# Optimization experiments

Measured on AMD Instinct MI355X. Metric: run time of the kernel, lower is better.

The kernel has to match this reference:

```python
import jax, jax.numpy as jnp
from jax import lax
import numpy as np

B, HI, WI = 8, 56, 56
HO, WO = HI // 2, WI // 2
DIN, DOUT = 96, 192
N_IN, N_OUT = HI * WI, HO * WO
HD = 32
NH = DOUT // HD
H2, W2, N2 = HO, WO, HO * WO
NA_W = 7
NUM_ITERS, DEPTH = 3, 2


def _build_group_tables():
    # M_loc: 0 inside 3x3 output window around each input token, -1e4 elsewhere
    # qidx: which of the 9 relative offsets maps (input i -> output j); -1 outside window
    mask = np.full((N_IN, N_OUT), -1e4, np.float32)
    idx = np.full((N_IN, N_OUT), -1, np.int64)
    rr, cc = np.meshgrid(np.arange(HI), np.arange(WI), indexing='ij')
    rr, cc = rr.ravel(), cc.ravel()
    r0, c0 = rr // 2, cc // 2
    ii = np.arange(N_IN)
    offs = [(dr, dc) for dr in (-1, 0, 1) for dc in (-1, 0, 1)]
    for kk, (dr, dc) in enumerate(offs):
        oi = np.clip(r0 + dr, 0, HO - 1) * WO + np.clip(c0 + dc, 0, WO - 1)
        mask[ii, oi] = 0.0
        idx[ii, oi] = kk
    # torch rpb[-1] == rpb[8]; emulate negative indexing with %9
    return jnp.asarray(mask), jnp.asarray(idx % 9)

M_LOC, QIDX = _build_group_tables()


def _rope_tables(n, d):
    inv = 1.0 / (10000.0 ** (np.arange(0, d, 2, dtype=np.float32) / d))
    ang = np.outer(np.arange(n, dtype=np.float32), inv)
    return jnp.asarray(np.cos(ang), jnp.float32), jnp.asarray(np.sin(ang), jnp.float32)

ROPE_COS, ROPE_SIN = _rope_tables(N2, HD)


def _na_idx(n, w):
    # NATTEN-style shifted windows: center clamped so the window stays in-bounds
    half = w // 2
    c = np.clip(np.arange(n), half, n - 1 - half)
    return jnp.asarray(c[:, None] + np.arange(-half, half + 1)[None, :])

NB_R = _na_idx(H2, NA_W)
NB_C = _na_idx(W2, NA_W)


def _ln(x, g, b):
    m = x.mean(-1, keepdims=True)
    v = ((x - m) ** 2).mean(-1, keepdims=True)
    return (x - m) / jnp.sqrt(v + 1e-5) * g + b


def _rope(t):  # t: [B, N, heads, head_dim]
    b, n, h, d = t.shape
    tr = t.reshape(b, n, h, d // 2, 2)
    x0, x1 = tr[..., 0], tr[..., 1]
    c = ROPE_COS[None, :, None, :]
    s = ROPE_SIN[None, :, None, :]
    return jnp.stack([x0 * c - x1 * s, x1 * c + x0 * s], -1).reshape(b, n, h, d)


def _forward(x, seed_conv_w, q_proj_w, k_proj_w, v_proj_w, g_ln_in_g, g_ln_in_b, g_ln_out_g, g_ln_out_b, g_ln_attn_g, g_ln_attn_b, g_ln_mlp_g, g_ln_mlp_b, g_mlp_w1, g_mlp_b1, g_mlp_w2, g_mlp_b2, tau, rpb, blk_ln1_g, blk_ln1_b, blk_ln2_g, blk_ln2_b, blk_qkv_w, blk_proj_w, blk_proj_b, blk_mlp_w1, blk_mlp_b1, blk_mlp_w2, blk_mlp_b2):
    b = x.shape[0]
    # ---- SparseGroupingLayer (local/sparse path), eval mode ----
    xc = x.transpose(0, 2, 1).reshape(b, DIN, HI, WI)
    seed = lax.conv_general_dilated(xc, seed_conv_w, (2, 2), ((1, 1), (1, 1)), dimension_numbers=('NCHW', 'OIHW', 'NCHW'))
    x_out = _ln(seed.reshape(b, DOUT, N_OUT).transpose(0, 2, 1), g_ln_out_g, g_ln_out_b)
    xn = _ln(x, g_ln_in_g, g_ln_in_b)
    k = xn @ k_proj_w.T
    v = xn @ v_proj_w.T
    bias = rpb[QIDX] + M_LOC  # [N_in, N_out]
    scale = jnp.exp(tau[0])
    for _ in range(NUM_ITERS):
        q = _ln(x_out, g_ln_out_g, g_ln_out_b) @ q_proj_w.T  # [B, N_out, dim_in]
        logits = jnp.einsum('bnd,bmd->bnm', k, q) * scale + bias[None]
        a_ups = jax.nn.softmax(logits, -1)
        a_down = a_ups / (a_ups.sum(1, keepdims=True) + 1e-8)
        upd = jnp.einsum('bnm,bnd->bmd', a_down, v)
        x_out = x_out + _ln(upd, g_ln_attn_g, g_ln_attn_b)
        h = jax.nn.gelu(x_out @ g_mlp_w1.T + g_mlp_b1, approximate=False) @ g_mlp_w2.T + g_mlp_b2
        x_out = x_out + _ln(h, g_ln_mlp_g, g_ln_mlp_b)
    # ---- SeNaTraBlocks: neighborhood attention (window=7) + RoPE, eval mode ----
    rows = NB_R[:, None, :, None]
    cols = NB_C[None, :, None, :]
    for i in range(DEPTH):
        xb = _ln(x_out, blk_ln1_g[i], blk_ln1_b[i])
        qkv = (xb @ blk_qkv_w[i].T).reshape(b, N2, 3, NH, HD)
        q = _rope(qkv[:, :, 0]).transpose(0, 2, 1, 3).reshape(b, NH, H2, W2, HD)
        kk = _rope(qkv[:, :, 1]).transpose(0, 2, 1, 3).reshape(b, NH, H2, W2, HD)
        vv = qkv[:, :, 2].transpose(0, 2, 1, 3).reshape(b, NH, H2, W2, HD)
        kn = kk[:, :, rows, cols].reshape(b, NH, H2, W2, NA_W * NA_W, HD)
        vn = vv[:, :, rows, cols].reshape(b, NH, H2, W2, NA_W * NA_W, HD)
        att = jnp.einsum('bhijd,bhijkd->bhijk', q, kn) * (HD ** -0.5)
        att = jax.nn.softmax(att, -1)
        o = jnp.einsum('bhijk,bhijkd->bhijd', att, vn)
        o = o.reshape(b, NH, N2, HD).transpose(0, 2, 1, 3).reshape(b, N2, DOUT)
        x_out = x_out + (o @ blk_proj_w[i].T + blk_proj_b[i])
        xb = _ln(x_out, blk_ln2_g[i], blk_ln2_b[i])
        h = jax.nn.gelu(xb @ blk_mlp_w1[i].T + blk_mlp_b1[i], approximate=False) @ blk_mlp_w2[i].T + blk_mlp_b2[i]
        x_out = x_out + h
    return x_out


def setup_inputs() -> dict:
    key = jax.random.key(0)
    ks = jax.random.split(key, 12)
    hid_g, hid_b = 2 * DOUT, 3 * DOUT
    def rn(k, shape, s=0.02):
        return jax.random.normal(k, shape, jnp.float32) * s
    return {
        'x': jax.random.normal(ks[0], (B, N_IN, DIN), jnp.float32),
        'seed_conv_w': rn(ks[1], (DOUT, DIN, 3, 3), 0.05),
        'q_proj_w': rn(ks[2], (DIN, DOUT)),
        'k_proj_w': rn(ks[3], (DIN, DIN)),
        'v_proj_w': rn(ks[4], (DOUT, DIN)),
        'g_ln_in_g': jnp.ones((DIN,), jnp.float32), 'g_ln_in_b': jnp.zeros((DIN,), jnp.float32),
        'g_ln_out_g': jnp.ones((DOUT,), jnp.float32), 'g_ln_out_b': jnp.zeros((DOUT,), jnp.float32),
        'g_ln_attn_g': jnp.ones((DOUT,), jnp.float32), 'g_ln_attn_b': jnp.zeros((DOUT,), jnp.float32),
        'g_ln_mlp_g': jnp.ones((DOUT,), jnp.float32), 'g_ln_mlp_b': jnp.zeros((DOUT,), jnp.float32),
        'g_mlp_w1': rn(ks[5], (hid_g, DOUT)), 'g_mlp_b1': jnp.zeros((hid_g,), jnp.float32),
        'g_mlp_w2': rn(ks[6], (DOUT, hid_g)), 'g_mlp_b2': jnp.zeros((DOUT,), jnp.float32),
        'tau': jnp.array([float(np.log(DIN ** -0.5))], jnp.float32),
        'rpb': rn(ks[7], (9,)),
        'blk_ln1_g': jnp.ones((DEPTH, DOUT), jnp.float32), 'blk_ln1_b': jnp.zeros((DEPTH, DOUT), jnp.float32),
        'blk_ln2_g': jnp.ones((DEPTH, DOUT), jnp.float32), 'blk_ln2_b': jnp.zeros((DEPTH, DOUT), jnp.float32),
        'blk_qkv_w': rn(ks[8], (DEPTH, 3 * DOUT, DOUT)),
        'blk_proj_w': rn(ks[9], (DEPTH, DOUT, DOUT)), 'blk_proj_b': jnp.zeros((DEPTH, DOUT), jnp.float32),
        'blk_mlp_w1': rn(ks[10], (DEPTH, hid_b, DOUT)), 'blk_mlp_b1': jnp.zeros((DEPTH, hid_b), jnp.float32),
        'blk_mlp_w2': rn(ks[11], (DEPTH, DOUT, hid_b)), 'blk_mlp_b2': jnp.zeros((DEPTH, DOUT), jnp.float32),
    }


def reference(x, seed_conv_w, q_proj_w, k_proj_w, v_proj_w, g_ln_in_g, g_ln_in_b, g_ln_out_g, g_ln_out_b, g_ln_attn_g, g_ln_attn_b, g_ln_mlp_g, g_ln_mlp_b, g_mlp_w1, g_mlp_b1, g_mlp_w2, g_mlp_b2, tau, rpb, blk_ln1_g, blk_ln1_b, blk_ln2_g, blk_ln2_b, blk_qkv_w, blk_proj_w, blk_proj_b, blk_mlp_w1, blk_mlp_b1, blk_mlp_w2, blk_mlp_b2):
    return _forward(x, seed_conv_w, q_proj_w, k_proj_w, v_proj_w, g_ln_in_g, g_ln_in_b, g_ln_out_g, g_ln_out_b, g_ln_attn_g, g_ln_attn_b, g_ln_mlp_g, g_ln_mlp_b, g_mlp_w1, g_mlp_b1, g_mlp_w2, g_mlp_b2, tau, rpb, blk_ln1_g, blk_ln1_b, blk_ln2_g, blk_ln2_b, blk_qkv_w, blk_proj_w, blk_proj_b, blk_mlp_w1, blk_mlp_b1, blk_mlp_w2, blk_mlp_b2)
```

## Files before the change

kernel.cpp:

```cpp
#include <hip/hip_runtime.h>
#include <hip/hip_bf16.h>

#define DEV __device__ __forceinline__

typedef __attribute__((ext_vector_type(8))) short short8;
typedef __attribute__((ext_vector_type(4))) float f32x4;

DEV unsigned short f2b(float f) {
  union { float f; unsigned u; } v; v.f = f;
  unsigned r = v.u + 0x7FFFu + ((v.u >> 16) & 1u);
  return (unsigned short)(r >> 16);
}
DEV float b2f16(unsigned short b) {
  union { unsigned u; float f; } v; v.u = ((unsigned)b) << 16;
  return v.f;
}
DEV void tsplit(float v, short& h, short& l) {
  union { float f; unsigned u; } c; c.f = v;
  unsigned short hu = (unsigned short)(c.u >> 16);
  union { unsigned u; float f; } hb; hb.u = (unsigned)hu << 16;
  union { float f; unsigned u; } c2; c2.f = v - hb.f;
  h = (short)hu; l = (short)(c2.u >> 16);
}

__global__ void k_castw(const float* __restrict__ s0, const float* __restrict__ s1,
    const float* __restrict__ s2, const float* __restrict__ s3,
    const float* __restrict__ s4, const float* __restrict__ s5,
    const float* __restrict__ s6, const float* __restrict__ s7,
    const float* __restrict__ s8, const float* __restrict__ s9,
    short* __restrict__ dh, short* __restrict__ dl) {
  int idx = blockIdx.x * 256 + threadIdx.x;
  if (idx >= 1096704) return;
  float v;
  if (idx < 165888) {
    int co = idx / 864, rem = idx % 864;
    int k9 = rem / 96, ci = rem % 96;
    v = s0[co * 864 + ci * 9 + k9];
  } else {
    const float* src; int base;
    if      (idx < 175104) { src = s1; base = 165888; }
    else if (idx < 193536) { src = s2; base = 175104; }
    else if (idx < 211968) { src = s3; base = 193536; }
    else if (idx < 285696) { src = s4; base = 211968; }
    else if (idx < 359424) { src = s5; base = 285696; }
    else if (idx < 580608) { src = s6; base = 359424; }
    else if (idx < 654336) { src = s7; base = 580608; }
    else if (idx < 875520) { src = s8; base = 654336; }
    else                   { src = s9; base = 875520; }
    v = src[idx - base];
  }
  unsigned short h = f2b(v);
  dh[idx] = (short)h;
  dl[idx] = (short)f2b(v - b2f16(h));
}

__global__ void k_rope(float* ct, float* st) {
  int idx = blockIdx.x * 256 + threadIdx.x;
  if (idx >= 784 * 16) return;
  int n = idx >> 4, j = idx & 15;
  float inv = powf(10000.f, -(float)(2 * j) / 32.f);
  float ang = (float)n * inv;
  ct[idx] = cosf(ang);
  st[idx] = sinf(ang);
}

template<int D>
__global__ __launch_bounds__(256) void k_lnstat(const float* __restrict__ in,
    float2* __restrict__ stats, int M) {
  int tok = blockIdx.x * 4 + (threadIdx.x >> 6);
  int l = threadIdx.x & 63;
  if (tok >= M) return;
  const float* row = in + (size_t)tok * D;
  constexpr int E = (D + 63) / 64;
  float s = 0.f, s2 = 0.f;
#pragma unroll
  for (int e = 0; e < E; ++e) {
    int i = e * 64 + l;
    float x = (i < D) ? row[i] : 0.f;
    s += x; s2 += x * x;
  }
  for (int off = 32; off; off >>= 1) { s += __shfl_xor(s, off); s2 += __shfl_xor(s2, off); }
  float mean = s / D, var = s2 / D - mean * mean;
  if (l == 0) stats[tok] = make_float2(mean, rsqrtf(var + 1e-5f));
}

template<int ADD>
__global__ __launch_bounds__(256) void k_ln_epi(const float* __restrict__ raw,
    const float* __restrict__ g, const float* __restrict__ b,
    float* __restrict__ out, float2* __restrict__ stats, int M) {
  int tok = blockIdx.x * 4 + (threadIdx.x >> 6);
  int l = threadIdx.x & 63;
  if (tok >= M) return;
  const float* row = raw + (size_t)tok * 192;
  float v[3];
  float s = 0.f, s2 = 0.f;
#pragma unroll
  for (int e = 0; e < 3; ++e) {
    float x = row[e * 64 + l];
    v[e] = x; s += x; s2 += x * x;
  }
  for (int off = 32; off; off >>= 1) { s += __shfl_xor(s, off); s2 += __shfl_xor(s2, off); }
  float mean = s / 192.f, var = s2 / 192.f - mean * mean;
  float rstd = rsqrtf(var + 1e-5f);
  float* orow = out + (size_t)tok * 192;
  float t = 0.f, t2 = 0.f;
#pragma unroll
  for (int e = 0; e < 3; ++e) {
    int i = e * 64 + l;
    float r = (v[e] - mean) * rstd * g[i] + b[i];
    float nv = ADD ? (orow[i] + r) : r;
    orow[i] = nv;
    t += nv; t2 += nv * nv;
  }
  for (int off = 32; off; off >>= 1) { t += __shfl_xor(t, off); t2 += __shfl_xor(t2, off); }
  float m2 = t / 192.f, v2 = t2 / 192.f - m2 * m2;
  if (l == 0) stats[tok] = make_float2(m2, rsqrtf(v2 + 1e-5f));
}

template<int EPI, int CONV, int LNS>
__global__ __launch_bounds__(128) void k_mgemm(
    const float* __restrict__ A, const short* __restrict__ WH,
    const short* __restrict__ WL, const float* __restrict__ bias,
    float* __restrict__ C, int M, int N, int K,
    const float2* __restrict__ lnstats, const float* __restrict__ lng,
    const float* __restrict__ lnb,
    const float* __restrict__ ct, const float* __restrict__ st,
    float* __restrict__ o1, float* __restrict__ o2, float* __restrict__ o3) {
  __shared__ short AsH[32][40], AsL[32][40];
  __shared__ short BsH[64][40], BsL[64][40];
  int t = threadIdx.x;
  int m0 = blockIdx.x * 32, n0 = blockIdx.y * 64;
  int sr = t >> 2, sq = (t & 3) * 8;
  int sr2 = t >> 1, sq2 = (t & 1) * 16;
  int lane = t & 63, w = t >> 6;
  int fr = lane & 15, fq = lane >> 4;
  float2 lst = make_float2(0.f, 1.f);
  if (LNS) lst = lnstats[m0 + sr];
  f32x4 acc[2][2];
#pragma unroll
  for (int i = 0; i < 2; ++i)
#pragma unroll
    for (int j = 0; j < 2; ++j) acc[i][j] = (f32x4){0.f, 0.f, 0.f, 0.f};

  for (int kt = 0; kt < K; kt += 32) {
    short8 vh, vl;
    if (CONV) {
      int m = m0 + sr;
      int b = m / 784, rm = m % 784, ho = rm / 28, wo = rm % 28;
      int k = kt + sq;
      int k9 = k / 96, ci0 = k % 96;
      int hi = 2 * ho - 1 + k9 / 3, wi = 2 * wo - 1 + k9 % 3;
      if (hi >= 0 && hi < 56 && wi >= 0 && wi < 56) {
        const float* src = &A[((size_t)b * 3136 + hi * 56 + wi) * 96 + ci0];
        float4 a0 = *(const float4*)src;
        float4 a1 = *(const float4*)(src + 4);
        float av[8] = {a0.x, a0.y, a0.z, a0.w, a1.x, a1.y, a1.z, a1.w};
#pragma unroll
        for (int j = 0; j < 8; ++j) { short h, l2; tsplit(av[j], h, l2); vh[j] = h; vl[j] = l2; }
      } else {
#pragma unroll
        for (int j = 0; j < 8; ++j) { vh[j] = 0; vl[j] = 0; }
      }
    } else {
      const float4 a0 = *(const float4*)&A[(size_t)(m0 + sr) * K + kt + sq];
      const float4 a1 = *(const float4*)&A[(size_t)(m0 + sr) * K + kt + sq + 4];
      float av[8] = {a0.x, a0.y, a0.z, a0.w, a1.x, a1.y, a1.z, a1.w};
#pragma unroll
      for (int j = 0; j < 8; ++j) {
        if (LNS) av[j] = (av[j] - lst.x) * lst.y * lng[kt + sq + j] + lnb[kt + sq + j];
        short h, l2; tsplit(av[j], h, l2); vh[j] = h; vl[j] = l2;
      }
    }
    *(short8*)&AsH[sr][sq] = vh;
    *(short8*)&AsL[sr][sq] = vl;
    {
      int n = n0 + sr2;
      if (n < N) {
        *(short8*)&BsH[sr2][sq2]     = *(const short8*)&WH[(size_t)n * K + kt + sq2];
        *(short8*)&BsH[sr2][sq2 + 8] = *(const short8*)&WH[(size_t)n * K + kt + sq2 + 8];
        *(short8*)&BsL[sr2][sq2]     = *(const short8*)&WL[(size_t)n * K + kt + sq2];
        *(short8*)&BsL[sr2][sq2 + 8] = *(const short8*)&WL[(size_t)n * K + kt + sq2 + 8];
      } else {
        short8 z = {0, 0, 0, 0, 0, 0, 0, 0};
        *(short8*)&BsH[sr2][sq2] = z; *(short8*)&BsH[sr2][sq2 + 8] = z;
        *(short8*)&BsL[sr2][sq2] = z; *(short8*)&BsL[sr2][sq2 + 8] = z;
      }
    }
    __syncthreads();
    short8 ah[2], al[2], bh[2], bl[2];
#pragma unroll
    for (int s = 0; s < 2; ++s) {
      ah[s] = *(const short8*)&AsH[s * 16 + fr][fq * 8];
      al[s] = *(const short8*)&AsL[s * 16 + fr][fq * 8];
      bh[s] = *(const short8*)&BsH[w * 32 + s * 16 + fr][fq * 8];
      bl[s] = *(const short8*)&BsL[w * 32 + s * 16 + fr][fq * 8];
    }
#pragma unroll
    for (int i = 0; i < 2; ++i)
#pragma unroll
      for (int j = 0; j < 2; ++j) {
        acc[i][j] = __builtin_amdgcn_mfma_f32_16x16x32_bf16(ah[i], bh[j], acc[i][j], 0, 0, 0);
        acc[i][j] = __builtin_amdgcn_mfma_f32_16x16x32_bf16(ah[i], bl[j], acc[i][j], 0, 0, 0);
        acc[i][j] = __builtin_amdgcn_mfma_f32_16x16x32_bf16(al[i], bh[j], acc[i][j], 0, 0, 0);
      }
    __syncthreads();
  }
#pragma unroll
  for (int i = 0; i < 2; ++i) {
#pragma unroll
    for (int j = 0; j < 2; ++j) {
      int n = n0 + w * 32 + j * 16 + fr;
#pragma unroll
      for (int r = 0; r < 4; ++r) {
        int m = m0 + i * 16 + fq * 4 + r;
        float v = acc[i][j][r];
        float pa = 0.f;
        if (EPI == 3) pa = __shfl_xor(v, 1);
        if (n >= N) continue;
        if (bias) v += bias[n];
        if (EPI == 1) v = 0.5f * v * (1.f + erff(v * 0.70710678118654752f));
        if (EPI == 3) {
          int sec = n / 192, d = n % 192, h = d / 32, dh = d % 32;
          int b = m / 784, mm = m % 784;
          float val;
          if (sec < 2) {
            int jj = dh >> 1;
            float cc = ct[mm * 16 + jj], ss = st[mm * 16 + jj];
            val = (dh & 1) ? (v * cc + pa * ss) : (v * cc - pa * ss);
          } else val = v;
          float* dst = (sec == 0) ? o1 : ((sec == 1) ? o2 : o3);
          dst[(((size_t)b * 6 + h) * 784 + mm) * 32 + dh] = val;
        } else if (EPI == 5) {
          if (n < 96) o1[(size_t)m * 96 + n] = v;
          else        o2[(size_t)m * 192 + (n - 96)] = v;
        } else if (EPI == 2) {
          C[(size_t)m * N + n] += v;
        } else {
          C[(size_t)m * N + n] = v;
        }
      }
    }
  }
}

__global__ __launch_bounds__(256) void k_pass1(const float* __restrict__ kk,
    const float* __restrict__ q, const float* __restrict__ rpb,
    const float* __restrict__ tau, float* __restrict__ M, float* __restrict__ Z) {
  int tok = blockIdx.x * 4 + (threadIdx.x >> 6);
  int l = threadIdx.x & 63;
  int b = tok / 3136, n = tok % 3136;
  int r = n / 56, c = n % 56, r0 = r >> 1, c0 = c >> 1;
  int oi[9]; bool keep[9];
#pragma unroll
  for (int kki = 0; kki < 9; ++kki) {
    int dr = kki / 3 - 1, dc = kki % 3 - 1;
    int rr = min(max(r0 + dr, 0), 27), cc = min(max(c0 + dc, 0), 27);
    oi[kki] = rr * 28 + cc;
  }
#pragma unroll
  for (int kki = 0; kki < 9; ++kki) {
    bool kp = true;
#pragma unroll
    for (int k2 = kki + 1; k2 < 9; ++k2) if (oi[k2] == oi[kki]) kp = false;
    keep[kki] = kp;
  }
  float scale = expf(tau[0]);
  const float* kr = kk + (size_t)tok * 96;
  float k0 = kr[l];
  float k1 = (l < 32) ? kr[64 + l] : 0.f;
  float lg[9];
  float mx = -1e30f;
#pragma unroll
  for (int kki = 0; kki < 9; ++kki) {
    if (keep[kki]) {
      const float* qr = q + ((size_t)b * 784 + oi[kki]) * 96;
      float part = k0 * qr[l];
      if (l < 32) part += k1 * qr[64 + l];
      for (int off = 32; off; off >>= 1) part += __shfl_xor(part, off);
      lg[kki] = part * scale + rpb[kki];
      mx = fmaxf(mx, lg[kki]);
    } else lg[kki] = -1e30f;
  }
  float z = 0.f;
#pragma unroll
  for (int kki = 0; kki < 9; ++kki) if (keep[kki]) z += expf(lg[kki] - mx);
  if (l == 0) { M[tok] = mx; Z[tok] = z; }
}

__global__ __launch_bounds__(192) void k_pass2(const float* __restrict__ kk,
    const float* __restrict__ q, const float* __restrict__ vv,
    const float* __restrict__ M, const float* __restrict__ Z,
    const float* __restrict__ rpb, const float* __restrict__ tau,
    const float* __restrict__ g, const float* __restrict__ bb, float* __restrict__ xout) {
  int bid = blockIdx.x;
  int blk = (bid & 7) * 784 + (bid >> 3);
  int b = blk / 784, m = blk % 784;
  int r2 = m / 28, c2 = m % 28;
  int r0lo = (r2 == 0) ? 0 : r2 - 1, r0hi = (r2 == 27) ? 27 : r2 + 1;
  int c0lo = (c2 == 0) ? 0 : c2 - 1, c0hi = (c2 == 27) ? 27 : c2 + 1;
  int nrow = 2 * (r0hi - r0lo + 1), ncol = 2 * (c0hi - c0lo + 1);
  int cnt = nrow * ncol;
  __shared__ float qm[96], p[36];
  __shared__ int nlist[36];
  __shared__ float2 red[192];
  int t = threadIdx.x;
  if (t < 96) qm[t] = q[(size_t)blk * 96 + t];
  __syncthreads();
  if (t < cnt) {
    int rr = 2 * r0lo + t / ncol, cc = 2 * c0lo + t % ncol;
    int n = rr * 56 + cc, rr0 = rr >> 1, cc0 = cc >> 1;
    int kkf = 0;
#pragma unroll
    for (int kki = 0; kki < 9; ++kki) {
      int dr = kki / 3 - 1, dc = kki % 3 - 1;
      int ra = min(max(rr0 + dr, 0), 27), ca = min(max(cc0 + dc, 0), 27);
      if (ra == r2 && ca == c2) kkf = kki;
    }
    const float* krow = kk + ((size_t)b * 3136 + n) * 96;
    float d = 0.f;
    for (int i = 0; i < 96; ++i) d += krow[i] * qm[i];
    float scale = expf(tau[0]);
    float lg = d * scale + rpb[kkf];
    size_t idn = (size_t)b * 3136 + n;
    p[t] = expf(lg - M[idn]) / Z[idn];
    nlist[t] = n;
  }
  __syncthreads();
  float denom = 0.f;
  for (int jn = 0; jn < cnt; ++jn) denom += p[jn];
  float acc = 0.f;
  for (int jn = 0; jn < cnt; ++jn)
    acc += p[jn] * vv[((size_t)b * 3136 + nlist[jn]) * 192 + t];
  float upd = acc / (denom + 1e-8f);
  red[t] = make_float2(upd, upd * upd);
  __syncthreads();
  for (int s = 128; s > 0; s >>= 1) {
    if (t < s && t + s < 192) { red[t].x += red[t + s].x; red[t].y += red[t + s].y; }
    __syncthreads();
  }
  float mean = red[0].x / 192.f, var = red[0].y / 192.f - mean * mean;
  float rstd = rsqrtf(var + 1e-5f);
  xout[(size_t)blk * 192 + t] += (upd - mean) * rstd * g[t] + bb[t];
}

__global__ __launch_bounds__(256) void k_attn(const float* __restrict__ q3,
    const float* __restrict__ k3, const float* __restrict__ v3, float* __restrict__ ob) {
  int bid = blockIdx.x;
  int swz = (bid & 7) * 1176 + (bid >> 3);
  int unit = swz * 4 + (threadIdx.x >> 6);
  int l = threadIdx.x & 63;
  int b = unit / (6 * 784), rem = unit % (6 * 784), h = rem / 784, m = rem % 784;
  int i = m / 28, j = m % 28;
  int ib = min(max(i, 3), 24) - 3, jb = min(max(j, 3), 24) - 3;
  size_t base = (size_t)(b * 6 + h) * 784 * 32;
  const float4* q4 = (const float4*)(q3 + base + (size_t)m * 32);
  float4 qv[8];
#pragma unroll
  for (int e = 0; e < 8; ++e) qv[e] = q4[e];
  float logit = -1e30f;
  if (l < 49) {
    int nk = (ib + l / 7) * 28 + (jb + l % 7);
    const float4* k4 = (const float4*)(k3 + base + (size_t)nk * 32);
    float a = 0.f;
#pragma unroll
    for (int e = 0; e < 8; ++e) {
      float4 kv = k4[e];
      a += qv[e].x * kv.x + qv[e].y * kv.y + qv[e].z * kv.z + qv[e].w * kv.w;
    }
    logit = a * 0.17677669529663687f;
  }
  float mx = logit;
  for (int off = 32; off; off >>= 1) mx = fmaxf(mx, __shfl_xor(mx, off));
  float p = (l < 49) ? expf(logit - mx) : 0.f;
  int half = l >> 5, d = l & 31;
  const float* vb = v3 + base + d;
  int rowbase = ib * 28 + jb;
  float accA = 0.f, accB = 0.f, psum = 0.f;
  int pbits = __float_as_int(p);
#pragma unroll
  for (int kk2 = 0; kk2 < 25; ++kk2) {
    const int k0c = kk2;
    const int k1c = (kk2 + 25 <= 48) ? kk2 + 25 : 48;
    float pk0 = __int_as_float(__builtin_amdgcn_readlane(pbits, k0c));
    float pk1 = (kk2 < 24) ? __int_as_float(__builtin_amdgcn_readlane(pbits, k1c)) : 0.f;
    const int c0 = (k0c / 7) * 28 + (k0c % 7);
    const int c1 = (k1c / 7) * 28 + (k1c % 7);
    float pk = half ? pk1 : pk0;
    int nk = rowbase + (half ? c1 : c0);
    psum += pk;
    float term = pk * vb[(size_t)nk * 32];
    if (kk2 & 1) accB += term; else accA += term;
  }
  float acc = accA + accB;
  acc += __shfl_xor(acc, 32);
  psum += __shfl_xor(psum, 32);
  if (l < 32)
    ob[(((size_t)b * 784 + m) * 6 + h) * 32 + l] = acc / psum;
}

extern "C" void kernel_launch(void* const* d_in, const int* in_sizes, int n_in,
                              void* d_out, int out_size, void* d_ws, size_t ws_size,
                              hipStream_t stream) {
  (void)in_sizes; (void)n_in; (void)out_size; (void)ws_size;
  const float* x        = (const float*)d_in[0];
  const float* convw    = (const float*)d_in[1];
  const float* qw       = (const float*)d_in[2];
  const float* kw       = (const float*)d_in[3];
  const float* vw       = (const float*)d_in[4];
  const float* ln_in_g  = (const float*)d_in[5];
  const float* ln_in_b  = (const float*)d_in[6];
  const float* ln_out_g = (const float*)d_in[7];
  const float* ln_out_b = (const float*)d_in[8];
  const float* ln_at_g  = (const float*)d_in[9];
  const float* ln_at_b  = (const float*)d_in[10];
  const float* ln_ml_g  = (const float*)d_in[11];
  const float* ln_ml_b  = (const float*)d_in[12];
  const float* gw1      = (const float*)d_in[13];
  const float* gb1      = (const float*)d_in[14];
  const float* gw2      = (const float*)d_in[15];
  const float* gb2      = (const float*)d_in[16];
  const float* tau      = (const float*)d_in[17];
  const float* rpb      = (const float*)d_in[18];
  const float* bln1g    = (const float*)d_in[19];
  const float* bln1b    = (const float*)d_in[20];
  const float* bln2g    = (const float*)d_in[21];
  const float* bln2b    = (const float*)d_in[22];
  const float* bqkvw    = (const float*)d_in[23];
  const float* bprojw   = (const float*)d_in[24];
  const float* bprojb   = (const float*)d_in[25];
  const float* bmw1     = (const float*)d_in[26];
  const float* bmb1     = (const float*)d_in[27];
  const float* bmw2     = (const float*)d_in[28];
  const float* bmb2     = (const float*)d_in[29];

  float* XOUT = (float*)d_out;

  float* W = (float*)d_ws;
  size_t off = 0;
  float* Kb    = W + off; off += (size_t)25088 * 96;
  float* Vb    = W + off; off += (size_t)25088 * 192;
  float* Qb    = W + off; off += (size_t)6272 * 96;
  float* Mb    = W + off; off += (size_t)25088;
  float* Zb    = W + off; off += (size_t)25088;
  float* H1    = W + off; off += (size_t)6272 * 576;
  float* T2    = W + off; off += (size_t)6272 * 192;
  float* CT    = W + off; off += (size_t)784 * 16;
  float* ST    = W + off; off += (size_t)784 * 16;
  float2* S96  = (float2*)(W + off); off += (size_t)25088 * 2;
  float2* S192 = (float2*)(W + off); off += (size_t)6272 * 2;
  short* WBH   = (short*)(W + off); off += (size_t)548352 + 16;
  short* WBL   = (short*)(W + off); off += (size_t)548352 + 16;
  const size_t O_c = 0, O_k = 165888, O_v = 175104, O_q = 193536,
               O_g1 = 211968, O_g2 = 285696, O_qkv = 359424, O_p = 580608,
               O_m1 = 654336, O_m2 = 875520;
  (void)O_v;
  float* CRAW = T2;
  float* Q3 = Kb;
  float* K3 = Kb + (size_t)1204224;
  float* V3 = Vb;
  float* OB = Vb + (size_t)1204224;

  k_castw<<<4284, 256, 0, stream>>>(convw, kw, vw, qw, gw1, gw2, bqkvw, bprojw,
                                    bmw1, bmw2, WBH, WBL);
  k_rope<<<49, 256, 0, stream>>>(CT, ST);

  k_mgemm<0, 1, 0><<<dim3(196, 3), 128, 0, stream>>>(x, WBH + O_c, WBL + O_c, nullptr,
      CRAW, 6272, 192, 864, nullptr, nullptr, nullptr,
      nullptr, nullptr, nullptr, nullptr, nullptr);
  k_ln_epi<0><<<1568, 256, 0, stream>>>(CRAW, ln_out_g, ln_out_b, XOUT, S192, 6272);

  k_lnstat<96><<<6272, 256, 0, stream>>>(x, S96, 25088);
  k_mgemm<5, 0, 1><<<dim3(784, 5), 128, 0, stream>>>(x, WBH + O_k, WBL + O_k, nullptr,
      nullptr, 25088, 288, 96, S96, ln_in_g, ln_in_b,
      nullptr, nullptr, Kb, Vb, nullptr);

  for (int it = 0; it < 3; ++it) {
    k_mgemm<0, 0, 1><<<dim3(196, 2), 128, 0, stream>>>(XOUT, WBH + O_q, WBL + O_q, nullptr,
        Qb, 6272, 96, 192, S192, ln_out_g, ln_out_b,
        nullptr, nullptr, nullptr, nullptr, nullptr);
    k_pass1<<<6272, 256, 0, stream>>>(Kb, Qb, rpb, tau, Mb, Zb);
    k_pass2<<<6272, 192, 0, stream>>>(Kb, Qb, Vb, Mb, Zb, rpb, tau, ln_at_g, ln_at_b, XOUT);
    k_mgemm<1, 0, 0><<<dim3(196, 6), 128, 0, stream>>>(XOUT, WBH + O_g1, WBL + O_g1, gb1,
        H1, 6272, 384, 192, nullptr, nullptr, nullptr,
        nullptr, nullptr, nullptr, nullptr, nullptr);
    k_mgemm<0, 0, 0><<<dim3(196, 3), 128, 0, stream>>>(H1, WBH + O_g2, WBL + O_g2, gb2,
        T2, 6272, 192, 384, nullptr, nullptr, nullptr,
        nullptr, nullptr, nullptr, nullptr, nullptr);
    k_ln_epi<1><<<1568, 256, 0, stream>>>(T2, ln_ml_g, ln_ml_b, XOUT, S192, 6272);
  }

  for (int i = 0; i < 2; ++i) {
    if (i == 1) k_lnstat<192><<<1568, 256, 0, stream>>>(XOUT, S192, 6272);
    k_mgemm<3, 0, 1><<<dim3(196, 9), 128, 0, stream>>>(XOUT, WBH + O_qkv + (size_t)i * 110592,
        WBL + O_qkv + (size_t)i * 110592, nullptr,
        nullptr, 6272, 576, 192, S192, bln1g + (size_t)i * 192, bln1b + (size_t)i * 192,
        CT, ST, Q3, K3, V3);
    k_attn<<<9408, 256, 0, stream>>>(Q3, K3, V3, OB);
    k_mgemm<2, 0, 0><<<dim3(196, 3), 128, 0, stream>>>(OB, WBH + O_p + (size_t)i * 36864,
        WBL + O_p + (size_t)i * 36864, bprojb + (size_t)i * 192,
        XOUT, 6272, 192, 192, nullptr, nullptr, nullptr,
        nullptr, nullptr, nullptr, nullptr, nullptr);
    k_lnstat<192><<<1568, 256, 0, stream>>>(XOUT, S192, 6272);
    k_mgemm<1, 0, 1><<<dim3(196, 9), 128, 0, stream>>>(XOUT, WBH + O_m1 + (size_t)i * 110592,
        WBL + O_m1 + (size_t)i * 110592, bmb1 + (size_t)i * 576,
        H1, 6272, 576, 192, S192, bln2g + (size_t)i * 192, bln2b + (size_t)i * 192,
        nullptr, nullptr, nullptr, nullptr, nullptr);
    k_mgemm<2, 0, 0><<<dim3(196, 3), 128, 0, stream>>>(H1, WBH + O_m2 + (size_t)i * 110592,
        WBL + O_m2 + (size_t)i * 110592, bmb2 + (size_t)i * 192,
        XOUT, 6272, 192, 576, nullptr, nullptr, nullptr,
        nullptr, nullptr, nullptr, nullptr, nullptr);
  }
}
```

Before: 619.9 us.

## Precompute bf16 hi/lo split activations in producer epilogues instead of GEMM prologues

```diff
diff --git a/kernel.cpp b/kernel.cpp
--- a/kernel.cpp
+++ b/kernel.cpp
@@ -65,29 +65,42 @@
 }
 
 template<int D>
-__global__ __launch_bounds__(256) void k_lnstat(const float* __restrict__ in,
-    float2* __restrict__ stats, int M) {
+__global__ __launch_bounds__(256) void k_lnsplit(const float* __restrict__ in,
+    const float* __restrict__ g, const float* __restrict__ b,
+    short* __restrict__ xh, short* __restrict__ xl, int M) {
   int tok = blockIdx.x * 4 + (threadIdx.x >> 6);
   int l = threadIdx.x & 63;
   if (tok >= M) return;
   const float* row = in + (size_t)tok * D;
   constexpr int E = (D + 63) / 64;
+  float v[E];
   float s = 0.f, s2 = 0.f;
 #pragma unroll
   for (int e = 0; e < E; ++e) {
     int i = e * 64 + l;
     float x = (i < D) ? row[i] : 0.f;
-    s += x; s2 += x * x;
+    v[e] = x; s += x; s2 += x * x;
   }
   for (int off = 32; off; off >>= 1) { s += __shfl_xor(s, off); s2 += __shfl_xor(s2, off); }
   float mean = s / D, var = s2 / D - mean * mean;
-  if (l == 0) stats[tok] = make_float2(mean, rsqrtf(var + 1e-5f));
+  float rstd = rsqrtf(var + 1e-5f);
+#pragma unroll
+  for (int e = 0; e < E; ++e) {
+    int i = e * 64 + l;
+    if (i < D) {
+      float r = (v[e] - mean) * rstd * g[i] + b[i];
+      short h2, l2; tsplit(r, h2, l2);
+      xh[(size_t)tok * D + i] = h2;
+      xl[(size_t)tok * D + i] = l2;
+    }
+  }
 }
 
 template<int ADD>
 __global__ __launch_bounds__(256) void k_ln_epi(const float* __restrict__ raw,
     const float* __restrict__ g, const float* __restrict__ b,
-    float* __restrict__ out, float2* __restrict__ stats, int M) {
+    const float* __restrict__ eg, const float* __restrict__ eb,
+    float* __restrict__ out, short* __restrict__ xh, short* __restrict__ xl, int M) {
   int tok = blockIdx.x * 4 + (threadIdx.x >> 6);
   int l = threadIdx.x & 63;
   if (tok >= M) return;
@@ -103,29 +116,39 @@
   float mean = s / 192.f, var = s2 / 192.f - mean * mean;
   float rstd = rsqrtf(var + 1e-5f);
   float* orow = out + (size_t)tok * 192;
+  float nv[3];
   float t = 0.f, t2 = 0.f;
 #pragma unroll
   for (int e = 0; e < 3; ++e) {
     int i = e * 64 + l;
     float r = (v[e] - mean) * rstd * g[i] + b[i];
-    float nv = ADD ? (orow[i] + r) : r;
-    orow[i] = nv;
-    t += nv; t2 += nv * nv;
+    float x = ADD ? (orow[i] + r) : r;
+    orow[i] = x;
+    nv[e] = x;
+    t += x; t2 += x * x;
   }
   for (int off = 32; off; off >>= 1) { t += __shfl_xor(t, off); t2 += __shfl_xor(t2, off); }
   float m2 = t / 192.f, v2 = t2 / 192.f - m2 * m2;
-  if (l == 0) stats[tok] = make_float2(m2, rsqrtf(v2 + 1e-5f));
-}
-
-template<int EPI, int CONV, int LNS>
+  float rstd2 = rsqrtf(v2 + 1e-5f);
+#pragma unroll
+  for (int e = 0; e < 3; ++e) {
+    int i = e * 64 + l;
+    float r = (nv[e] - m2) * rstd2 * eg[i] + eb[i];
+    short h2, l2; tsplit(r, h2, l2);
+    xh[(size_t)tok * 192 + i] = h2;
+    xl[(size_t)tok * 192 + i] = l2;
+  }
+}
+
+template<int EPI, int SRC>
 __global__ __launch_bounds__(128) void k_mgemm(
-    const float* __restrict__ A, const short* __restrict__ WH,
+    const float* __restrict__ Aconv, const short* __restrict__ AH,
+    const short* __restrict__ AL, const short* __restrict__ WH,
     const short* __restrict__ WL, const float* __restrict__ bias,
     float* __restrict__ C, int M, int N, int K,
-    const float2* __restrict__ lnstats, const float* __restrict__ lng,
-    const float* __restrict__ lnb,
     const float* __restrict__ ct, const float* __restrict__ st,
-    float* __restrict__ o1, float* __restrict__ o2, float* __restrict__ o3) {
+    float* __restrict__ o1, float* __restrict__ o2, float* __restrict__ o3,
+    short* __restrict__ oh, short* __restrict__ ol) {
   __shared__ short AsH[32][40], AsL[32][40];
   __shared__ short BsH[64][40], BsL[64][40];
   int t = threadIdx.x;
@@ -134,8 +157,6 @@
   int sr2 = t >> 1, sq2 = (t & 1) * 16;
   int lane = t & 63, w = t >> 6;
   int fr = lane & 15, fq = lane >> 4;
-  float2 lst = make_float2(0.f, 1.f);
-  if (LNS) lst = lnstats[m0 + sr];
   f32x4 acc[2][2];
 #pragma unroll
   for (int i = 0; i < 2; ++i)
@@ -143,15 +164,18 @@
     for (int j = 0; j < 2; ++j) acc[i][j] = (f32x4){0.f, 0.f, 0.f, 0.f};
 
   for (int kt = 0; kt < K; kt += 32) {
-    short8 vh, vl;
-    if (CONV) {
+    if (SRC == 1) {
+      *(short8*)&AsH[sr][sq] = *(const short8*)&AH[(size_t)(m0 + sr) * K + kt + sq];
+      *(short8*)&AsL[sr][sq] = *(const short8*)&AL[(size_t)(m0 + sr) * K + kt + sq];
+    } else {
+      short8 vh, vl;
       int m = m0 + sr;
       int b = m / 784, rm = m % 784, ho = rm / 28, wo = rm % 28;
       int k = kt + sq;
       int k9 = k / 96, ci0 = k % 96;
       int hi = 2 * ho - 1 + k9 / 3, wi = 2 * wo - 1 + k9 % 3;
       if (hi >= 0 && hi < 56 && wi >= 0 && wi < 56) {
-        const float* src = &A[((size_t)b * 3136 + hi * 56 + wi) * 96 + ci0];
+        const float* src = &Aconv[((size_t)b * 3136 + hi * 56 + wi) * 96 + ci0];
         float4 a0 = *(const float4*)src;
         float4 a1 = *(const float4*)(src + 4);
         float av[8] = {a0.x, a0.y, a0.z, a0.w, a1.x, a1.y, a1.z, a1.w};
@@ -161,18 +185,9 @@
 #pragma unroll
         for (int j = 0; j < 8; ++j) { vh[j] = 0; vl[j] = 0; }
       }
-    } else {
-      const float4 a0 = *(const float4*)&A[(size_t)(m0 + sr) * K + kt + sq];
-      const float4 a1 = *(const float4*)&A[(size_t)(m0 + sr) * K + kt + sq + 4];
-      float av[8] = {a0.x, a0.y, a0.z, a0.w, a1.x, a1.y, a1.z, a1.w};
-#pragma unroll
-      for (int j = 0; j < 8; ++j) {
-        if (LNS) av[j] = (av[j] - lst.x) * lst.y * lng[kt + sq + j] + lnb[kt + sq + j];
-        short h, l2; tsplit(av[j], h, l2); vh[j] = h; vl[j] = l2;
-      }
-    }
-    *(short8*)&AsH[sr][sq] = vh;
-    *(short8*)&AsL[sr][sq] = vl;
+      *(short8*)&AsH[sr][sq] = vh;
+      *(short8*)&AsL[sr][sq] = vl;
+    }
     {
       int n = n0 + sr2;
       if (n < N) {
@@ -218,8 +233,12 @@
         if (EPI == 3) pa = __shfl_xor(v, 1);
         if (n >= N) continue;
         if (bias) v += bias[n];
-        if (EPI == 1) v = 0.5f * v * (1.f + erff(v * 0.70710678118654752f));
-        if (EPI == 3) {
+        if (EPI == 1) {
+          v = 0.5f * v * (1.f + erff(v * 0.70710678118654752f));
+          short h2, l2; tsplit(v, h2, l2);
+          oh[(size_t)m * N + n] = h2;
+          ol[(size_t)m * N + n] = l2;
+        } else if (EPI == 3) {
           int sec = n / 192, d = n % 192, h = d / 32, dh = d % 32;
           int b = m / 784, mm = m % 784;
           float val;
@@ -291,7 +310,8 @@
     const float* __restrict__ q, const float* __restrict__ vv,
     const float* __restrict__ M, const float* __restrict__ Z,
     const float* __restrict__ rpb, const float* __restrict__ tau,
-    const float* __restrict__ g, const float* __restrict__ bb, float* __restrict__ xout) {
+    const float* __restrict__ g, const float* __restrict__ bb,
+    float* __restrict__ xout, short* __restrict__ xh, short* __restrict__ xl) {
   int bid = blockIdx.x;
   int blk = (bid & 7) * 784 + (bid >> 3);
   int b = blk / 784, m = blk % 784;
@@ -340,11 +360,16 @@
   }
   float mean = red[0].x / 192.f, var = red[0].y / 192.f - mean * mean;
   float rstd = rsqrtf(var + 1e-5f);
-  xout[(size_t)blk * 192 + t] += (upd - mean) * rstd * g[t] + bb[t];
+  float nv = xout[(size_t)blk * 192 + t] + (upd - mean) * rstd * g[t] + bb[t];
+  xout[(size_t)blk * 192 + t] = nv;
+  short h2, l2; tsplit(nv, h2, l2);
+  xh[(size_t)blk * 192 + t] = h2;
+  xl[(size_t)blk * 192 + t] = l2;
 }
 
 __global__ __launch_bounds__(256) void k_attn(const float* __restrict__ q3,
-    const float* __restrict__ k3, const float* __restrict__ v3, float* __restrict__ ob) {
+    const float* __restrict__ k3, const float* __restrict__ v3,
+    short* __restrict__ obh, short* __restrict__ obl) {
   int bid = blockIdx.x;
   int swz = (bid & 7) * 1176 + (bid >> 3);
   int unit = swz * 4 + (threadIdx.x >> 6);
@@ -394,8 +419,13 @@
   float acc = accA + accB;
   acc += __shfl_xor(acc, 32);
   psum += __shfl_xor(psum, 32);
-  if (l < 32)
-    ob[(((size_t)b * 784 + m) * 6 + h) * 32 + l] = acc / psum;
+  if (l < 32) {
+    float o = acc / psum;
+    short h2, l2; tsplit(o, h2, l2);
+    size_t idx = (((size_t)b * 784 + m) * 6 + h) * 32 + l;
+    obh[idx] = h2;
+    obl[idx] = l2;
+  }
 }
 
 extern "C" void kernel_launch(void* const* d_in, const int* in_sizes, int n_in,
@@ -442,72 +472,82 @@
   float* Qb    = W + off; off += (size_t)6272 * 96;
   float* Mb    = W + off; off += (size_t)25088;
   float* Zb    = W + off; off += (size_t)25088;
-  float* H1    = W + off; off += (size_t)6272 * 576;
   float* T2    = W + off; off += (size_t)6272 * 192;
   float* CT    = W + off; off += (size_t)784 * 16;
   float* ST    = W + off; off += (size_t)784 * 16;
-  float2* S96  = (float2*)(W + off); off += (size_t)25088 * 2;
-  float2* S192 = (float2*)(W + off); off += (size_t)6272 * 2;
+  short* XH96  = (short*)(W + off); off += (size_t)25088 * 96 / 2;
+  short* XL96  = (short*)(W + off); off += (size_t)25088 * 96 / 2;
+  short* XH    = (short*)(W + off); off += (size_t)6272 * 192 / 2;
+  short* XL    = (short*)(W + off); off += (size_t)6272 * 192 / 2;
+  short* H1H   = (short*)(W + off); off += (size_t)6272 * 576 / 2;
+  short* H1L   = (short*)(W + off); off += (size_t)6272 * 576 / 2;
+  short* OBH   = (short*)(W + off); off += (size_t)6272 * 192 / 2;
+  short* OBL   = (short*)(W + off); off += (size_t)6272 * 192 / 2;
   short* WBH   = (short*)(W + off); off += (size_t)548352 + 16;
   short* WBL   = (short*)(W + off); off += (size_t)548352 + 16;
-  const size_t O_c = 0, O_k = 165888, O_v = 175104, O_q = 193536,
+  const size_t O_c = 0, O_k = 165888, O_q = 193536,
                O_g1 = 211968, O_g2 = 285696, O_qkv = 359424, O_p = 580608,
                O_m1 = 654336, O_m2 = 875520;
-  (void)O_v;
   float* CRAW = T2;
   float* Q3 = Kb;
   float* K3 = Kb + (size_t)1204224;
   float* V3 = Vb;
-  float* OB = Vb + (size_t)1204224;
 
   k_castw<<<4284, 256, 0, stream>>>(convw, kw, vw, qw, gw1, gw2, bqkvw, bprojw,
                                     bmw1, bmw2, WBH, WBL);
   k_rope<<<49, 256, 0, stream>>>(CT, ST);
 
-  k_mgemm<0, 1, 0><<<dim3(196, 3), 128, 0, stream>>>(x, WBH + O_c, WBL + O_c, nullptr,
-      CRAW, 6272, 192, 864, nullptr, nullptr, nullptr,
-      nullptr, nullptr, nullptr, nullptr, nullptr);
-  k_ln_epi<0><<<1568, 256, 0, stream>>>(CRAW, ln_out_g, ln_out_b, XOUT, S192, 6272);
-
-  k_lnstat<96><<<6272, 256, 0, stream>>>(x, S96, 25088);
-  k_mgemm<5, 0, 1><<<dim3(784, 5), 128, 0, stream>>>(x, WBH + O_k, WBL + O_k, nullptr,
-      nullptr, 25088, 288, 96, S96, ln_in_g, ln_in_b,
-      nullptr, nullptr, Kb, Vb, nullptr);
+  k_mgemm<0, 0><<<dim3(196, 3), 128, 0, stream>>>(x, nullptr, nullptr,
+      WBH + O_c, WBL + O_c, nullptr, CRAW, 6272, 192, 864,
+      nullptr, nullptr, nullptr, nullptr, nullptr, nullptr, nullptr);
+  k_ln_epi<0><<<1568, 256, 0, stream>>>(CRAW, ln_out_g, ln_out_b, ln_out_g, ln_out_b,
+                                        XOUT, XH, XL, 6272);
+
+  k_lnsplit<96><<<6272, 256, 0, stream>>>(x, ln_in_g, ln_in_b, XH96, XL96, 25088);
+  k_mgemm<5, 1><<<dim3(784, 5), 128, 0, stream>>>(nullptr, XH96, XL96,
+      WBH + O_k, WBL + O_k, nullptr, nullptr, 25088, 288, 96,
+      nullptr, nullptr, Kb, Vb, nullptr, nullptr, nullptr);
 
   for (int it = 0; it < 3; ++it) {
-    k_mgemm<0, 0, 1><<<dim3(196, 2), 128, 0, stream>>>(XOUT, WBH + O_q, WBL + O_q, nullptr,
-        Qb, 6272, 96, 192, S192, ln_out_g, ln_out_b,
-        nullptr, nullptr, nullptr, nullptr, nullptr);
+    k_mgemm<0, 1><<<dim3(196, 2), 128, 0, stream>>>(nullptr, XH, XL,
+        WBH + O_q, WBL + O_q, nullptr, Qb, 6272, 96, 192,
+        nullptr, nullptr, nullptr, nullptr, nullptr, nullptr, nullptr);
     k_pass1<<<6272, 256, 0, stream>>>(Kb, Qb, rpb, tau, Mb, Zb);
-    k_pass2<<<6272, 192, 0, stream>>>(Kb, Qb, Vb, Mb, Zb, rpb, tau, ln_at_g, ln_at_b, XOUT);
-    k_mgemm<1, 0, 0><<<dim3(196, 6), 128, 0, stream>>>(XOUT, WBH + O_g1, WBL + O_g1, gb1,
-        H1, 6272, 384, 192, nullptr, nullptr, nullptr,
-        nullptr, nullptr, nullptr, nullptr, nullptr);
-    k_mgemm<0, 0, 0><<<dim3(196, 3), 128, 0, stream>>>(H1, WBH + O_g2, WBL + O_g2, gb2,
-        T2, 6272, 192, 384, nullptr, nullptr, nullptr,
-        nullptr, nullptr, nullptr, nullptr, nullptr);
-    k_ln_epi<1><<<1568, 256, 0, stream>>>(T2, ln_ml_g, ln_ml_b, XOUT, S192, 6272);
+    k_pass2<<<6272, 192, 0, stream>>>(Kb, Qb, Vb, Mb, Zb, rpb, tau, ln_at_g, ln_at_b,
+                                      XOUT, XH, XL);
+    k_mgemm<1, 1><<<dim3(196, 6), 128, 0, stream>>>(nullptr, XH, XL,
+        WBH + O_g1, WBL + O_g1, gb1, nullptr, 6272, 384, 192,
+        nullptr, nullptr, nullptr, nullptr, nullptr, H1H, H1L);
+    k_mgemm<0, 1><<<dim3(196, 3), 128, 0, stream>>>(nullptr, H1H, H1L,
+        WBH + O_g2, WBL + O_g2, gb2, T2, 6272, 192, 384,
+        nullptr, nullptr, nullptr, nullptr, nullptr, nullptr, nullptr);
+    const float* eg = (it < 2) ? ln_out_g : bln1g;
+    const float* eb = (it < 2) ? ln_out_b : bln1b;
+    k_ln_epi<1><<<1568, 256, 0, stream>>>(T2, ln_ml_g, ln_ml_b, eg, eb,
+                                          XOUT, XH, XL, 6272);
   }
 
   for (int i = 0; i < 2; ++i) {
-    if (i == 1) k_lnstat<192><<<1568, 256, 0, stream>>>(XOUT, S192, 6272);
-    k_mgemm<3, 0, 1><<<dim3(196, 9), 128, 0, stream>>>(XOUT, WBH + O_qkv + (size_t)i * 110592,
-        WBL + O_qkv + (size_t)i * 110592, nullptr,
-        nullptr, 6272, 576, 192, S192, bln1g + (size_t)i * 192, bln1b + (size_t)i * 192,
-        CT, ST, Q3, K3, V3);
-    k_attn<<<9408, 256, 0, stream>>>(Q3, K3, V3, OB);
-    k_mgemm<2, 0, 0><<<dim3(196, 3), 128, 0, stream>>>(OB, WBH + O_p + (size_t)i * 36864,
-        WBL + O_p + (size_t)i * 36864, bprojb + (size_t)i * 192,
-        XOUT, 6272, 192, 192, nullptr, nullptr, nullptr,
-        nullptr, nullptr, nullptr, nullptr, nullptr);
-    k_lnstat<192><<<1568, 256, 0, stream>>>(XOUT, S192, 6272);
-    k_mgemm<1, 0, 1><<<dim3(196, 9), 128, 0, stream>>>(XOUT, WBH + O_m1 + (size_t)i * 110592,
-        WBL + O_m1 + (size_t)i * 110592, bmb1 + (size_t)i * 576,
-        H1, 6272, 576, 192, S192, bln2g + (size_t)i * 192, bln2b + (size_t)i * 192,
-        nullptr, nullptr, nullptr, nullptr, nullptr);
-    k_mgemm<2, 0, 0><<<dim3(196, 3), 128, 0, stream>>>(H1, WBH + O_m2 + (size_t)i * 110592,
-        WBL + O_m2 + (size_t)i * 110592, bmb2 + (size_t)i * 192,
-        XOUT, 6272, 192, 576, nullptr, nullptr, nullptr,
-        nullptr, nullptr, nullptr, nullptr, nullptr);
-  }
-}
+    k_mgemm<3, 1><<<dim3(196, 9), 128, 0, stream>>>(nullptr, XH, XL,
+        WBH + O_qkv + (size_t)i * 110592, WBL + O_qkv + (size_t)i * 110592, nullptr,
+        nullptr, 6272, 576, 192, CT, ST, Q3, K3, V3, nullptr, nullptr);
+    k_attn<<<9408, 256, 0, stream>>>(Q3, K3, V3, OBH, OBL);
+    k_mgemm<2, 1><<<dim3(196, 3), 128, 0, stream>>>(nullptr, OBH, OBL,
+        WBH + O_p + (size_t)i * 36864, WBL + O_p + (size_t)i * 36864,
+        bprojb + (size_t)i * 192, XOUT, 6272, 192, 192,
+        nullptr, nullptr, nullptr, nullptr, nullptr, nullptr, nullptr);
+    k_lnsplit<192><<<1568, 256, 0, stream>>>(XOUT, bln2g + (size_t)i * 192,
+        bln2b + (size_t)i * 192, XH, XL, 6272);
+    k_mgemm<1, 1><<<dim3(196, 9), 128, 0, stream>>>(nullptr, XH, XL,
+        WBH + O_m1 + (size_t)i * 110592, WBL + O_m1 + (size_t)i * 110592,
+        bmb1 + (size_t)i * 576, nullptr, 6272, 576, 192,
+        nullptr, nullptr, nullptr, nullptr, nullptr, H1H, H1L);
+    k_mgemm<2, 1><<<dim3(196, 3), 128, 0, stream>>>(nullptr, H1H, H1L,
+        WBH + O_m2 + (size_t)i * 110592, WBL + O_m2 + (size_t)i * 110592,
+        bmb2 + (size_t)i * 192, XOUT, 6272, 192, 576,
+        nullptr, nullptr, nullptr, nullptr, nullptr, nullptr, nullptr);
+    if (i == 0)
+      k_lnsplit<192><<<1568, 256, 0, stream>>>(XOUT, bln1g + 192, bln1b + 192,
+                                               XH, XL, 6272);
+  }
+}
```

Result: no change. 615.1 us (-0.8%).
